# Performance work log

Hardware: AMD Instinct MI355X
Metric: run time of the kernel (lower is better)

The kernel has to match this reference:

```python
import jax, jax.numpy as jnp
import numpy as np


def setup_inputs() -> dict:
    key = jax.random.key(0)
    ks = jax.random.split(key, 6)
    b, h, t, dh = 8, 8, 8192, 64
    buckets = 128
    return {
        "q": jax.random.normal(ks[0], (b, h, t, dh), jnp.float32),
        "k": jax.random.normal(ks[1], (b, h, t, dh), jnp.float32),
        "v": jax.random.normal(ks[2], (b, h, t, dh), jnp.float32),
        "sort_W": jax.random.normal(ks[3], (1, h, 2 * dh, buckets + 1), jnp.float32),
        "null_keys": jax.random.normal(ks[4], (h, 1, dh), jnp.float32),
        "null_values": jax.random.normal(ks[5], (h, 1, dh), jnp.float32),
    }


def _sinkhorn_causal_attention(q, k, v, sort_W, null_keys, null_values):
    b, h, t, dh = q.shape
    buckets = sort_W.shape[-1] - 1
    d = h * dh  # full model dim; torch code scales by d**-0.5 (not d_h)
    bsz = t // buckets
    hh = h // 2
    bh = b * h

    # rotate second half of heads left by bsz-1 along time
    def rot_heads(x, shift):
        return jnp.concatenate([x[:, :hh], jnp.roll(x[:, hh:], shift, axis=2)], axis=1)

    q = rot_heads(q, -(bsz - 1))
    k = rot_heads(k, -(bsz - 1))
    v = rot_heads(v, -(bsz - 1))

    qf = q.reshape(bh, t, dh)
    kf = k.reshape(bh, t, dh)
    vf = v.reshape(bh, t, dh)
    b_q = qf.reshape(bh, buckets, bsz, dh)
    b_k = kf.reshape(bh, buckets, bsz, dh)
    b_v = vf.reshape(bh, buckets, bsz, dh)

    # ---- CausalSimpleSortNet ----
    denom = jnp.arange(1, t + 1, dtype=kf.dtype)[None, :, None]
    k_cum = jnp.cumsum(kf, axis=1) / denom                      # cumavg over time
    k_r = jnp.concatenate([k_cum, kf], axis=-1)                  # [bh, t, 2dh]
    x = k_r.reshape(bh, buckets, bsz, 2 * dh)[:, :, 0]           # first token of each bucket
    R = jnp.einsum('bhud,hdc->bhuc', x.reshape(b, h, buckets, 2 * dh), sort_W[0])
    R = jax.nn.leaky_relu(R).reshape(bh, buckets, buckets + 1)

    # mask_reordering_matrix: forbid current/future buckets, softmax, strict lower-tri
    rows = jnp.arange(buckets)[:, None]
    cols = jnp.arange(buckets + 1)[None, :]
    neg = -jnp.finfo(R.dtype).max
    R = jnp.where(cols >= rows + 1, neg, R)
    R = jax.nn.softmax(R, axis=-1)
    R = jnp.where(cols < rows, R, jnp.zeros((), R.dtype))

    # zero_all_but_top (k=1) along last dim
    top_idx = jnp.argmax(R, axis=-1)                             # [bh, buckets]
    top_mask = cols[None] == top_idx[..., None]
    R = jnp.where(top_mask, R, jnp.zeros((), R.dtype))

    # null bucket prepended to keys/values
    b_null_k = jnp.broadcast_to(null_keys[None, :, None], (b, h, 1, bsz, dh)).reshape(bh, 1, bsz, dh)
    b_null_v = jnp.broadcast_to(null_values[None, :, None], (b, h, 1, bsz, dh)).reshape(bh, 1, bsz, dh)
    b_k_full = jnp.concatenate([b_null_k, b_k], axis=1)          # [bh, buckets+1, bsz, dh]
    b_v_full = jnp.concatenate([b_null_v, b_v], axis=1)

    # soft gather of routed buckets
    b_k_r = jnp.einsum('buv,bvtd->butd', R, b_k_full)
    b_v_r = jnp.einsum('buv,bvtd->butd', R, b_v_full)
    b_k2 = jnp.concatenate([b_k_r, b_k], axis=2)                 # [bh, buckets, 2bsz, dh]
    b_v2 = jnp.concatenate([b_v_r, b_v], axis=2)

    dots = jnp.einsum('buie,buje->buij', b_q, b_k2) * (d ** -0.5)

    # attention mask
    i = jnp.arange(bsz)[:, None]
    j = jnp.arange(bsz)[None, :]
    base = jnp.concatenate([jnp.ones((bsz, bsz), bool), j <= i], axis=-1)  # [bsz, 2bsz]
    head_rot = (jnp.arange(h) >= hh)[None, :, None, None, None]
    last_bkt = (jnp.arange(buckets) == buckets - 1)[None, None, :, None, None]
    row_idx = jnp.arange(bsz)[None, None, None, :, None]
    col_idx = jnp.arange(2 * bsz)[None, None, None, None, :]
    special = (col_idx <= bsz) & (row_idx >= 1)
    mask = base[None, None, None] & ~(head_rot & last_bkt & special)
    mask = jnp.broadcast_to(mask, (b, h, buckets, bsz, 2 * bsz)).reshape(bh, buckets, bsz, 2 * bsz)

    dots = jnp.where(mask, dots, -jnp.finfo(dots.dtype).max)
    attn = jax.nn.softmax(dots, axis=-1)
    out = jnp.einsum('buij,buje->buie', attn, b_v2)              # [bh, buckets, bsz, dh]
    out = out.reshape(b, h, t, dh)
    out = jnp.concatenate([out[:, :hh], jnp.roll(out[:, hh:], bsz - 1, axis=2)], axis=1)
    return out


def reference(q, k, v, sort_W, null_keys, null_values):
    return _sinkhorn_causal_attention(q, k, v, sort_W, null_keys, null_values)
```

## Files before the change

### kernel.cpp

```cpp
#include <hip/hip_runtime.h>

#define T     8192
#define DH    64
#define TMASK 8191
#define SCALE 0.044194173824159216f
#define NEGF  -3.402823466e38f

typedef __attribute__((ext_vector_type(8))) short bf16x8;
typedef __attribute__((ext_vector_type(4))) float f32x4;

static __device__ __forceinline__ unsigned short f2bf(float f) {
  unsigned int u = __float_as_uint(f);
  u += 0x7fffu + ((u >> 16) & 1u);
  return (unsigned short)(u >> 16);
}

__global__ void __launch_bounds__(256) seg_sums_kernel(
    const float* __restrict__ k, float* __restrict__ segs) {
  int bid = blockIdx.x;
  int bhi = bid >> 3;
  int ch  = bid & 7;
  int hd  = bhi & 7;
  bool rot = hd >= 4;
  int tid = threadIdx.x;
  int lane = tid & 63;
  int wv   = tid >> 6;
  int sg   = ch * 16 + wv * 4 + (lane >> 4);
  int c4   = (lane & 15) << 2;
  const float* kb = k + (size_t)bhi * T * DH;
  int t0 = sg * 64;
  float s0 = 0.f, s1 = 0.f, s2 = 0.f, s3 = 0.f;
#pragma unroll 8
  for (int s = 0; s < 64; ++s) {
    int t  = t0 + s;
    int st = rot ? ((t + 63) & TMASK) : t;
    float4 x = *(const float4*)(kb + (size_t)st * DH + c4);
    s0 += x.x; s1 += x.y; s2 += x.z; s3 += x.w;
  }
  *(float4*)(segs + ((size_t)bhi * 128 + sg) * 64 + c4) =
      make_float4(s0, s1, s2, s3);
}

__global__ void __launch_bounds__(256) route_kernel(
    const float* __restrict__ k, const float* __restrict__ sortW,
    const float* __restrict__ segs,
    int* __restrict__ routeIdx, float* __restrict__ routeP) {
  __shared__ float sSeg[128 * 64];
  __shared__ float sX[16 * 128];
  int bid = blockIdx.x;
  int bhi = bid >> 3;
  int u0  = (bid & 7) * 16;
  int hd  = bhi & 7;
  bool rot = hd >= 4;
  int tid = threadIdx.x;
  const float* kb = k + (size_t)bhi * T * DH;
  const float* sg = segs + (size_t)bhi * 128 * 64;

#pragma unroll
  for (int it = 0; it < 8; ++it) {
    int f4 = (it * 256 + tid) * 4;
    *(float4*)(sSeg + f4) = *(const float4*)(sg + f4);
  }
  {
    int r = tid >> 4, c4 = (tid & 15) << 2;
    int t = (u0 + r) * 64;
    int st = rot ? ((t + 63) & TMASK) : t;
    *(float4*)(sX + r * 128 + 64 + c4) = *(const float4*)(kb + (size_t)st * DH + c4);
  }
  __syncthreads();
  {
    int r = tid >> 4, c4 = (tid & 15) << 2;
    int u = u0 + r;
    float4 run = make_float4(0.f, 0.f, 0.f, 0.f);
    for (int uu = 0; uu < u; ++uu) {
      float4 sv = *(const float4*)(sSeg + uu * 64 + c4);
      run.x += sv.x; run.y += sv.y; run.z += sv.z; run.w += sv.w;
    }
    float4 first = *(const float4*)(sX + r * 128 + 64 + c4);
    float den = (float)(u * 64 + 1);
    float4 cum = make_float4((run.x + first.x) / den, (run.y + first.y) / den,
                             (run.z + first.z) / den, (run.w + first.w) / den);
    *(float4*)(sX + r * 128 + c4) = cum;
  }
  __syncthreads();

  int ty = tid >> 4, tx = tid & 15;
  int u = u0 + ty;
  const float* Wh = sortW + (size_t)hd * 128 * 129;
  float z[8] = {0.f, 0.f, 0.f, 0.f, 0.f, 0.f, 0.f, 0.f};
#pragma unroll 4
  for (int d = 0; d < 128; ++d) {
    float xv = sX[ty * 128 + d];
    const float* wr = Wh + (size_t)d * 129 + tx;
#pragma unroll
    for (int j = 0; j < 8; ++j) z[j] = fmaf(xv, wr[j * 16], z[j]);
  }
  float l[8];
  float mx = NEGF;
#pragma unroll
  for (int j = 0; j < 8; ++j) {
    int c = tx + 16 * j;
    float lv = z[j] >= 0.f ? z[j] : 0.01f * z[j];
    l[j] = lv;
    if (c <= u) mx = fmaxf(mx, lv);
  }
  for (int off = 1; off < 16; off <<= 1) mx = fmaxf(mx, __shfl_xor(mx, off));
  float se = 0.f;
#pragma unroll
  for (int j = 0; j < 8; ++j) {
    int c = tx + 16 * j;
    if (c <= u) se += __expf(l[j] - mx);
  }
  for (int off = 1; off < 16; off <<= 1) se += __shfl_xor(se, off);
  float bv = NEGF; int bi = 0x7fffffff;
#pragma unroll
  for (int j = 0; j < 8; ++j) {
    int c = tx + 16 * j;
    if (c < u && (l[j] > bv || (l[j] == bv && c < bi))) { bv = l[j]; bi = c; }
  }
  for (int off = 1; off < 16; off <<= 1) {
    float ov = __shfl_xor(bv, off); int oi = __shfl_xor(bi, off);
    if (ov > bv || (ov == bv && oi < bi)) { bv = ov; bi = oi; }
  }
  if (tx == 0) {
    if (u == 0) { routeIdx[bhi * 128] = 0; routeP[bhi * 128] = 0.f; }
    else {
      routeIdx[bhi * 128 + u] = bi;
      routeP[bhi * 128 + u]   = __expf(bv - mx) / se;
    }
  }
}

__global__ void __launch_bounds__(256, 4) attn_kernel(
    const float* __restrict__ q, const float* __restrict__ k,
    const float* __restrict__ v,
    const float* __restrict__ nullk, const float* __restrict__ nullv,
    const int* __restrict__ routeIdx, const float* __restrict__ routeP,
    float* __restrict__ out) {
  __shared__ __align__(16) unsigned short smem[17408];
  unsigned short* sK  = smem;
  unsigned short* sVt = smem + 9216;
  unsigned short* sP  = smem;

  const int bid0 = blockIdx.x;
  const int bid  = ((bid0 & 7) << 10) | (bid0 >> 3);
  const int u   = bid & 127;
  const int bhi = bid >> 7;
  const int hd  = bhi & 7;
  const bool rot = hd >= 4;
  const int tid = threadIdx.x;
  const float* qb = q + (size_t)bhi * T * DH;
  const float* kb = k + (size_t)bhi * T * DH;
  const float* vb = v + (size_t)bhi * T * DH;
  float* ob = out + (size_t)bhi * T * DH;
  const int   ridx = routeIdx[bhi * 128 + u];
  const float p    = routeP[bhi * 128 + u];
  const float* nkh = nullk + hd * DH;
  const float* nvh = nullv + hd * DH;

  const int lane = tid & 63;
  const int w    = tid >> 6;
  const int col  = lane & 15;
  const int quad = lane >> 4;
  const int kofs = quad * 8;
  const int mrow = w * 16 + col;

  bf16x8 aq0, aq1;
  {
    int t  = u * 64 + mrow;
    int st = rot ? ((t + 63) & TMASK) : t;
    const float* qr = qb + (size_t)st * DH + kofs;
    float4 a0 = *(const float4*)(qr + 0);
    float4 a1 = *(const float4*)(qr + 4);
    float4 a2 = *(const float4*)(qr + 32);
    float4 a3 = *(const float4*)(qr + 36);
    aq0[0] = (short)f2bf(a0.x * SCALE); aq0[1] = (short)f2bf(a0.y * SCALE);
    aq0[2] = (short)f2bf(a0.z * SCALE); aq0[3] = (short)f2bf(a0.w * SCALE);
    aq0[4] = (short)f2bf(a1.x * SCALE); aq0[5] = (short)f2bf(a1.y * SCALE);
    aq0[6] = (short)f2bf(a1.z * SCALE); aq0[7] = (short)f2bf(a1.w * SCALE);
    aq1[0] = (short)f2bf(a2.x * SCALE); aq1[1] = (short)f2bf(a2.y * SCALE);
    aq1[2] = (short)f2bf(a2.z * SCALE); aq1[3] = (short)f2bf(a2.w * SCALE);
    aq1[4] = (short)f2bf(a3.x * SCALE); aq1[5] = (short)f2bf(a3.y * SCALE);
    aq1[6] = (short)f2bf(a3.z * SCALE); aq1[7] = (short)f2bf(a3.w * SCALE);
  }

#pragma unroll
  for (int it = 0; it < 8; ++it) {
    int flat = it * 256 + tid;
    int row = flat >> 4, c4 = (flat & 15) << 2;
    float4 kv;
    if (row < 64) {
      if (ridx == 0) kv = *(const float4*)(nkh + c4);
      else {
        int t = (ridx - 1) * 64 + row;
        int st = rot ? ((t + 63) & TMASK) : t;
        kv = *(const float4*)(kb + (size_t)st * DH + c4);
      }
      kv.x *= p; kv.y *= p; kv.z *= p; kv.w *= p;
    } else {
      int t = u * 64 + (row - 64);
      int st = rot ? ((t + 63) & TMASK) : t;
      kv = *(const float4*)(kb + (size_t)st * DH + c4);
    }
    ushort4 o4;
    o4.x = f2bf(kv.x); o4.y = f2bf(kv.y); o4.z = f2bf(kv.z); o4.w = f2bf(kv.w);
    *(ushort4*)(sK + row * 72 + c4) = o4;
  }

#pragma unroll
  for (int it = 0; it < 2; ++it) {
    int flat = it * 256 + tid;
    int tok4 = flat >> 4;
    int d4   = (flat & 15) << 2;
    int tb   = tok4 * 4;
    float va[4][4];
    if (tb < 64) {
      if (ridx == 0) {
        float4 nv = *(const float4*)(nvh + d4);
        float n0 = nv.x * p, n1 = nv.y * p, n2 = nv.z * p, n3 = nv.w * p;
#pragma unroll
        for (int jj = 0; jj < 4; ++jj) {
          va[jj][0] = n0; va[jj][1] = n1; va[jj][2] = n2; va[jj][3] = n3;
        }
      } else {
#pragma unroll
        for (int jj = 0; jj < 4; ++jj) {
          int t = (ridx - 1) * 64 + tb + jj;
          int st = rot ? ((t + 63) & TMASK) : t;
          float4 x = *(const float4*)(vb + (size_t)st * DH + d4);
          va[jj][0] = x.x * p; va[jj][1] = x.y * p;
          va[jj][2] = x.z * p; va[jj][3] = x.w * p;
        }
      }
    } else {
#pragma unroll
      for (int jj = 0; jj < 4; ++jj) {
        int t = u * 64 + (tb - 64) + jj;
        int st = rot ? ((t + 63) & TMASK) : t;
        float4 x = *(const float4*)(vb + (size_t)st * DH + d4);
        va[jj][0] = x.x; va[jj][1] = x.y; va[jj][2] = x.z; va[jj][3] = x.w;
      }
    }
    int chunk = tok4 >> 1, ph = tok4 & 1;
#pragma unroll
    for (int dd = 0; dd < 4; ++dd) {
      int n = d4 + dd;
      ushort4 o;
      o.x = f2bf(va[0][dd]); o.y = f2bf(va[1][dd]);
      o.z = f2bf(va[2][dd]); o.w = f2bf(va[3][dd]);
      *(ushort4*)(sVt + n * 128 + ((chunk ^ (n & 15)) << 3) + (ph << 2)) = o;
    }
  }
  __syncthreads();

  f32x4 acc[8];
#pragma unroll
  for (int j = 0; j < 8; ++j) acc[j] = (f32x4){0.f, 0.f, 0.f, 0.f};
#pragma unroll
  for (int j = 0; j < 8; ++j) {
    bf16x8 b0 = *(const bf16x8*)(sK + (j * 16 + col) * 72 + 0  + kofs);
    acc[j] = __builtin_amdgcn_mfma_f32_16x16x32_bf16(aq0, b0, acc[j], 0, 0, 0);
    bf16x8 b1 = *(const bf16x8*)(sK + (j * 16 + col) * 72 + 32 + kofs);
    acc[j] = __builtin_amdgcn_mfma_f32_16x16x32_bf16(aq1, b1, acc[j], 0, 0, 0);
  }

  const bool spec = rot && (u == 127);
#pragma unroll
  for (int reg = 0; reg < 4; ++reg) {
    int r = w * 16 + quad * 4 + reg;
    float mx = -1e30f;
#pragma unroll
    for (int j = 0; j < 8; ++j) {
      int c = j * 16 + col;
      bool vis = (c < 64) || ((c - 64) <= r);
      if (spec && r >= 1 && c <= 64) vis = false;
      float val = vis ? acc[j][reg] : -1e30f;
      acc[j][reg] = val;
      mx = fmaxf(mx, val);
    }
#pragma unroll
    for (int off = 1; off < 16; off <<= 1) mx = fmaxf(mx, __shfl_xor(mx, off));
    float s = 0.f;
#pragma unroll
    for (int j = 0; j < 8; ++j) {
      float e = __expf(acc[j][reg] - mx);
      acc[j][reg] = e; s += e;
    }
#pragma unroll
    for (int off = 1; off < 16; off <<= 1) s += __shfl_xor(s, off);
    float inv = 1.f / s;
#pragma unroll
    for (int j = 0; j < 8; ++j) acc[j][reg] *= inv;
  }

  __syncthreads();
#pragma unroll
  for (int j = 0; j < 8; ++j) {
#pragma unroll
    for (int reg = 0; reg < 4; ++reg) {
      unsigned int mybf = f2bf(acc[j][reg]);
      unsigned int obf  = (unsigned int)__shfl_xor((int)mybf, 1);
      if ((col & 1) == 0) {
        int r = w * 16 + quad * 4 + reg;
        *(unsigned int*)(sP + r * 136 + j * 16 + col) = mybf | (obf << 16);
      }
    }
  }
  __syncthreads();

  f32x4 oacc[4];
#pragma unroll
  for (int jt = 0; jt < 4; ++jt) oacc[jt] = (f32x4){0.f, 0.f, 0.f, 0.f};
#pragma unroll
  for (int ks = 0; ks < 4; ++ks) {
    bf16x8 ap = *(const bf16x8*)(sP + mrow * 136 + ks * 32 + kofs);
#pragma unroll
    for (int jt = 0; jt < 4; ++jt) {
      int n = jt * 16 + col;
      bf16x8 bv = *(const bf16x8*)(sVt + n * 128 + (((ks * 4 + quad) ^ col) << 3));
      oacc[jt] = __builtin_amdgcn_mfma_f32_16x16x32_bf16(ap, bv, oacc[jt], 0, 0, 0);
    }
  }

#pragma unroll
  for (int reg = 0; reg < 4; ++reg) {
    int r = w * 16 + quad * 4 + reg;
    int t = u * 64 + r;
    int st = rot ? ((t + 63) & TMASK) : t;
    float* orow = ob + (size_t)st * DH;
#pragma unroll
    for (int jt = 0; jt < 4; ++jt)
      orow[jt * 16 + col] = oacc[jt][reg];
  }
}

extern "C" void kernel_launch(void* const* d_in, const int* in_sizes, int n_in,
                              void* d_out, int out_size, void* d_ws, size_t ws_size,
                              hipStream_t stream) {
  const float* q     = (const float*)d_in[0];
  const float* k     = (const float*)d_in[1];
  const float* v     = (const float*)d_in[2];
  const float* sortW = (const float*)d_in[3];
  const float* nullk = (const float*)d_in[4];
  const float* nullv = (const float*)d_in[5];
  float* out = (float*)d_out;

  float* segs     = (float*)d_ws;
  int*   routeIdx = (int*)((char*)d_ws + (size_t)64 * 128 * 64 * 4);
  float* routeP   = (float*)((char*)d_ws + (size_t)64 * 128 * 64 * 4 + 32768);

  seg_sums_kernel<<<512, 256, 0, stream>>>(k, segs);
  route_kernel<<<512, 256, 0, stream>>>(k, sortW, segs, routeIdx, routeP);
  attn_kernel<<<8192, 256, 0, stream>>>(q, k, v, nullk, nullv,
                                        routeIdx, routeP, out);
}
```

Measured before the change: 454.6 us.

## Swizzle LDS layouts, defer softmax normalization, transpose PV MFMA for vector stores

Replaces padded K and P shared-memory rows with XOR-swizzled unpadded layouts, which shrinks LDS and allows raising the occupancy hint from 4 to 5 blocks. Uses the hardware bf16 conversion and packed pair writes instead of manual rounding. Moves the softmax division to after the PV product by swapping the MFMA operands so each lane holds four consecutive output columns, giving float4 global stores scaled by a broadcast reciprocal. Also simplifies mask evaluation. Risks include register pressure under the tighter launch bound and small numeric differences from using unnormalized P in bf16.

Result: no change. 453.5 us (-0.3%).

```diff
diff --git a/kernel.cpp b/kernel.cpp
--- a/kernel.cpp
+++ b/kernel.cpp
@@ -8,11 +8,14 @@
 
 typedef __attribute__((ext_vector_type(8))) short bf16x8;
 typedef __attribute__((ext_vector_type(4))) float f32x4;
+typedef __attribute__((ext_vector_type(4))) unsigned int u32x4;
 
 static __device__ __forceinline__ unsigned short f2bf(float f) {
-  unsigned int u = __float_as_uint(f);
-  u += 0x7fffu + ((u >> 16) & 1u);
-  return (unsigned short)(u >> 16);
+  __bf16 h = (__bf16)f;
+  return __builtin_bit_cast(unsigned short, h);
+}
+static __device__ __forceinline__ unsigned int pk2(float a, float b) {
+  return (unsigned int)f2bf(a) | ((unsigned int)f2bf(b) << 16);
 }
 
 __global__ void __launch_bounds__(256) seg_sums_kernel(
@@ -131,15 +134,15 @@
   }
 }
 
-__global__ void __launch_bounds__(256, 4) attn_kernel(
+__global__ void __launch_bounds__(256, 5) attn_kernel(
     const float* __restrict__ q, const float* __restrict__ k,
     const float* __restrict__ v,
     const float* __restrict__ nullk, const float* __restrict__ nullv,
     const int* __restrict__ routeIdx, const float* __restrict__ routeP,
     float* __restrict__ out) {
-  __shared__ __align__(16) unsigned short smem[17408];
+  __shared__ __align__(16) unsigned short smem[16384];
   unsigned short* sK  = smem;
-  unsigned short* sVt = smem + 9216;
+  unsigned short* sVt = smem + 8192;
   unsigned short* sP  = smem;
 
   const int bid0 = blockIdx.x;
@@ -174,14 +177,17 @@
     float4 a1 = *(const float4*)(qr + 4);
     float4 a2 = *(const float4*)(qr + 32);
     float4 a3 = *(const float4*)(qr + 36);
-    aq0[0] = (short)f2bf(a0.x * SCALE); aq0[1] = (short)f2bf(a0.y * SCALE);
-    aq0[2] = (short)f2bf(a0.z * SCALE); aq0[3] = (short)f2bf(a0.w * SCALE);
-    aq0[4] = (short)f2bf(a1.x * SCALE); aq0[5] = (short)f2bf(a1.y * SCALE);
-    aq0[6] = (short)f2bf(a1.z * SCALE); aq0[7] = (short)f2bf(a1.w * SCALE);
-    aq1[0] = (short)f2bf(a2.x * SCALE); aq1[1] = (short)f2bf(a2.y * SCALE);
-    aq1[2] = (short)f2bf(a2.z * SCALE); aq1[3] = (short)f2bf(a2.w * SCALE);
-    aq1[4] = (short)f2bf(a3.x * SCALE); aq1[5] = (short)f2bf(a3.y * SCALE);
-    aq1[6] = (short)f2bf(a3.z * SCALE); aq1[7] = (short)f2bf(a3.w * SCALE);
+    u32x4 t0, t1;
+    t0[0] = pk2(a0.x * SCALE, a0.y * SCALE);
+    t0[1] = pk2(a0.z * SCALE, a0.w * SCALE);
+    t0[2] = pk2(a1.x * SCALE, a1.y * SCALE);
+    t0[3] = pk2(a1.z * SCALE, a1.w * SCALE);
+    t1[0] = pk2(a2.x * SCALE, a2.y * SCALE);
+    t1[1] = pk2(a2.z * SCALE, a2.w * SCALE);
+    t1[2] = pk2(a3.x * SCALE, a3.y * SCALE);
+    t1[3] = pk2(a3.z * SCALE, a3.w * SCALE);
+    aq0 = __builtin_bit_cast(bf16x8, t0);
+    aq1 = __builtin_bit_cast(bf16x8, t1);
   }
 
 #pragma unroll
@@ -202,9 +208,10 @@
       int st = rot ? ((t + 63) & TMASK) : t;
       kv = *(const float4*)(kb + (size_t)st * DH + c4);
     }
-    ushort4 o4;
-    o4.x = f2bf(kv.x); o4.y = f2bf(kv.y); o4.z = f2bf(kv.z); o4.w = f2bf(kv.w);
-    *(ushort4*)(sK + row * 72 + c4) = o4;
+    uint2 o;
+    o.x = pk2(kv.x, kv.y);
+    o.y = pk2(kv.z, kv.w);
+    *(uint2*)(sK + row * 64 + (((c4 >> 3) ^ (row & 7)) << 3) + (c4 & 7)) = o;
   }
 
 #pragma unroll
@@ -245,36 +252,46 @@
 #pragma unroll
     for (int dd = 0; dd < 4; ++dd) {
       int n = d4 + dd;
-      ushort4 o;
-      o.x = f2bf(va[0][dd]); o.y = f2bf(va[1][dd]);
-      o.z = f2bf(va[2][dd]); o.w = f2bf(va[3][dd]);
-      *(ushort4*)(sVt + n * 128 + ((chunk ^ (n & 15)) << 3) + (ph << 2)) = o;
-    }
-  }
-  __syncthreads();
-
+      uint2 o;
+      o.x = pk2(va[0][dd], va[1][dd]);
+      o.y = pk2(va[2][dd], va[3][dd]);
+      *(uint2*)(sVt + n * 128 + ((chunk ^ (n & 15)) << 3) + (ph << 2)) = o;
+    }
+  }
+  __syncthreads();
+
+  const int kx0 = ((quad ^ (col & 7)) << 3);
+  const int kx1 = (((4 + quad) ^ (col & 7)) << 3);
   f32x4 acc[8];
 #pragma unroll
   for (int j = 0; j < 8; ++j) acc[j] = (f32x4){0.f, 0.f, 0.f, 0.f};
 #pragma unroll
   for (int j = 0; j < 8; ++j) {
-    bf16x8 b0 = *(const bf16x8*)(sK + (j * 16 + col) * 72 + 0  + kofs);
+    int rowb = (j * 16 + col) * 64;
+    bf16x8 b0 = *(const bf16x8*)(sK + rowb + kx0);
     acc[j] = __builtin_amdgcn_mfma_f32_16x16x32_bf16(aq0, b0, acc[j], 0, 0, 0);
-    bf16x8 b1 = *(const bf16x8*)(sK + (j * 16 + col) * 72 + 32 + kofs);
+    bf16x8 b1 = *(const bf16x8*)(sK + rowb + kx1);
     acc[j] = __builtin_amdgcn_mfma_f32_16x16x32_bf16(aq1, b1, acc[j], 0, 0, 0);
   }
 
   const bool spec = rot && (u == 127);
+  float s4[4];
 #pragma unroll
   for (int reg = 0; reg < 4; ++reg) {
     int r = w * 16 + quad * 4 + reg;
+    bool killLow = spec && (r >= 1);
     float mx = -1e30f;
 #pragma unroll
     for (int j = 0; j < 8; ++j) {
-      int c = j * 16 + col;
-      bool vis = (c < 64) || ((c - 64) <= r);
-      if (spec && r >= 1 && c <= 64) vis = false;
-      float val = vis ? acc[j][reg] : -1e30f;
+      float val = acc[j][reg];
+      if (j < 4) {
+        if (killLow) val = -1e30f;
+      } else {
+        int cc = (j - 4) * 16 + col;
+        bool vis = cc <= r;
+        if (j == 4) vis = vis && !(killLow && col == 0);
+        if (!vis) val = -1e30f;
+      }
       acc[j][reg] = val;
       mx = fmaxf(mx, val);
     }
@@ -288,9 +305,7 @@
     }
 #pragma unroll
     for (int off = 1; off < 16; off <<= 1) s += __shfl_xor(s, off);
-    float inv = 1.f / s;
-#pragma unroll
-    for (int j = 0; j < 8; ++j) acc[j][reg] *= inv;
+    s4[reg] = s;
   }
 
   __syncthreads();
@@ -298,11 +313,11 @@
   for (int j = 0; j < 8; ++j) {
 #pragma unroll
     for (int reg = 0; reg < 4; ++reg) {
-      unsigned int mybf = f2bf(acc[j][reg]);
-      unsigned int obf  = (unsigned int)__shfl_xor((int)mybf, 1);
+      float partner = __shfl_xor(acc[j][reg], 1);
       if ((col & 1) == 0) {
         int r = w * 16 + quad * 4 + reg;
-        *(unsigned int*)(sP + r * 136 + j * 16 + col) = mybf | (obf << 16);
+        int phys = r * 128 + ((((2 * j) + (col >> 3)) ^ (r & 15)) << 3) + (col & 7);
+        *(unsigned int*)(sP + phys) = pk2(acc[j][reg], partner);
       }
     }
   }
@@ -313,24 +328,35 @@
   for (int jt = 0; jt < 4; ++jt) oacc[jt] = (f32x4){0.f, 0.f, 0.f, 0.f};
 #pragma unroll
   for (int ks = 0; ks < 4; ++ks) {
-    bf16x8 ap = *(const bf16x8*)(sP + mrow * 136 + ks * 32 + kofs);
+    int slot = (((ks * 4 + quad) ^ col) << 3);
+    bf16x8 ap = *(const bf16x8*)(sP + mrow * 128 + slot);
 #pragma unroll
     for (int jt = 0; jt < 4; ++jt) {
       int n = jt * 16 + col;
-      bf16x8 bv = *(const bf16x8*)(sVt + n * 128 + (((ks * 4 + quad) ^ col) << 3));
-      oacc[jt] = __builtin_amdgcn_mfma_f32_16x16x32_bf16(ap, bv, oacc[jt], 0, 0, 0);
-    }
-  }
-
-#pragma unroll
-  for (int reg = 0; reg < 4; ++reg) {
-    int r = w * 16 + quad * 4 + reg;
-    int t = u * 64 + r;
+      bf16x8 bv = *(const bf16x8*)(sVt + n * 128 + slot);
+      oacc[jt] = __builtin_amdgcn_mfma_f32_16x16x32_bf16(bv, ap, oacc[jt], 0, 0, 0);
+    }
+  }
+
+  int srcl = (col >> 2) << 4;
+  float sv0 = __shfl(s4[0], srcl);
+  float sv1 = __shfl(s4[1], srcl);
+  float sv2 = __shfl(s4[2], srcl);
+  float sv3 = __shfl(s4[3], srcl);
+  float sa = (col & 1) ? sv1 : sv0;
+  float sb = (col & 1) ? sv3 : sv2;
+  float invR = __builtin_amdgcn_rcpf((col & 2) ? sb : sa);
+
+  {
+    int t = u * 64 + mrow;
     int st = rot ? ((t + 63) & TMASK) : t;
-    float* orow = ob + (size_t)st * DH;
-#pragma unroll
-    for (int jt = 0; jt < 4; ++jt)
-      orow[jt * 16 + col] = oacc[jt][reg];
+    float* orow = ob + (size_t)st * DH + quad * 4;
+#pragma unroll
+    for (int jt = 0; jt < 4; ++jt) {
+      float4 o4 = make_float4(oacc[jt][0] * invR, oacc[jt][1] * invR,
+                              oacc[jt][2] * invR, oacc[jt][3] * invR);
+      *(float4*)(orow + jt * 16) = o4;
+    }
   }
 }
 
```
